# Optimization experiments

Measured on AMD Instinct MI355X. Metric: run time of the kernel, lower is better.

The kernel has to match this reference:

```python
import jax, jax.numpy as jnp
import numpy as np

B, L, H, D_IN = 64, 4096, 128, 3

def setup_inputs() -> dict:
    key = jax.random.key(0)
    ks = jax.random.split(key, 9)
    def lin_w(k, fan_in, shape):
        bound = 1.0 / np.sqrt(fan_in)
        return jax.random.uniform(k, shape, jnp.float32, -bound, bound)
    return {
        "x": jax.random.normal(ks[0], (B, L, D_IN), jnp.float32),
        "Wp": lin_w(ks[1], D_IN, (D_IN, H)), "bp": lin_w(ks[2], D_IN, (H,)),
        "Wz": lin_w(ks[3], H, (H, H)),      "bz": lin_w(ks[4], H, (H,)),
        "Wh": lin_w(ks[5], H, (H, H)),      "bh": lin_w(ks[6], H, (H,)),
        "Wg": lin_w(ks[7], H, (H, 1)),      "bg": lin_w(ks[8], H, (1,)),
    }

def reference(x, Wp, bp, Wz, bz, Wh, bh, Wg, bg):
    # Batched projections across all timesteps (B, L, H)
    inp = x @ Wp + bp                      # input_proj
    z = jax.nn.sigmoid(inp @ Wz + bz)      # update gate
    h_tilde = jnp.tanh(inp @ Wh + bh)      # candidate
    # Linear recurrence h_t = a_t * h_{t-1} + b_t, h_{-1} = 0
    a = 1.0 - z
    b = z * h_tilde
    def combine(c1, c2):
        a1, b1 = c1
        a2, b2 = c2
        return (a1 * a2, b1 * a2 + b2)
    _, h = jax.lax.associative_scan(combine, (a, b), axis=1)  # h_t (since h_{-1}=0)
    # Readout uses h BEFORE the update at each step: preds_t = gauss_head(h_{t-1})
    h_prev = jnp.concatenate([jnp.zeros_like(h[:, :1]), h[:, :-1]], axis=1)
    preds = h_prev @ Wg + bg               # (B, L, 1)
    return preds
```

## Files before the change

kernel.cpp:

```cpp
#include <hip/hip_runtime.h>
#include <hip/hip_bf16.h>
#include <stdint.h>

#define B_   64
#define L_   4096
#define H_   128
#define T_   64
#define C_   (L_/T_)
#define BH_  (B_*H_)
#define PADI 136

typedef __attribute__((ext_vector_type(8))) short short8;
typedef __attribute__((ext_vector_type(4))) short short4v;
typedef __attribute__((ext_vector_type(4))) float floatx4;
typedef __attribute__((ext_vector_type(2))) float floatx2;

#define LOG2E 1.44269504088896340736f

__device__ __forceinline__ unsigned short f2bf(float f){
    unsigned int u = __float_as_uint(f);
    u += 0x7FFFu + ((u >> 16) & 1u);
    return (unsigned short)(u >> 16);
}
__device__ __forceinline__ float bf2f(unsigned short s){
    return __uint_as_float(((unsigned int)s) << 16);
}

__global__ void prep_w(const float* __restrict__ Wz, const float* __restrict__ Wh,
                       unsigned short* __restrict__ WzT, unsigned short* __restrict__ WhT){
    int b = blockIdx.x;
    const float* W = (b < 16) ? Wz : Wh;
    unsigned short* WT = (b < 16) ? WzT : WhT;
    int b16 = b & 15, tid = threadIdx.x;
    #pragma unroll
    for (int it = 0; it < 4; ++it){
        int idx = b16*1024 + it*256 + tid;
        int n = idx >> 7, k = idx & 127;
        WT[idx] = f2bf(W[k*H_ + n]);
    }
}

__global__ __launch_bounds__(256, 4)
void carry_kogge(const floatx2* __restrict__ agg2, float* __restrict__ carry_g){
    const int row  = blockIdx.x*4 + (threadIdx.x >> 6);
    const int lane = threadIdx.x & 63;
    floatx2 v = agg2[(size_t)row*C_ + lane];
    #pragma unroll
    for (int d = 1; d < 64; d <<= 1){
        float oA = __shfl_up(v[0], d, 64);
        float oH = __shfl_up(v[1], d, 64);
        if (lane >= d){
            v[1] = fmaf(oH, v[0], v[1]);
            v[0] = oA * v[0];
        }
    }
    float eh = __shfl_up(v[1], 1, 64);
    carry_g[(size_t)row*C_ + lane] = (lane == 0) ? 0.0f : eh;
}


__global__ __launch_bounds__(256, 4)
void gates_agg(const float* __restrict__ x,
               const float* __restrict__ Wp, const float* __restrict__ bp,
               const float* __restrict__ bz, const float* __restrict__ bh,
               const float* __restrict__ Wg,
               const unsigned short* __restrict__ WzT,
               const unsigned short* __restrict__ WhT,
               floatx2* __restrict__ agg2,
               float* __restrict__ sloc, unsigned short* __restrict__ pw_g)
{
    __shared__ __align__(16) unsigned short s_ab[H_*H_];
    __shared__ float s_bz[H_], s_bh[H_], s_wg[H_];
    __shared__ float s_part[256];
    unsigned short* inp_lds = s_ab;

    const int bid = blockIdx.x;
    const int bb  = bid / C_;
    const int cc  = bid % C_;
    const int t0g = cc * T_;
    const int tid = threadIdx.x;
    const int wv = tid >> 6, lane = tid & 63, quad = lane >> 4, l15 = lane & 15;

    if (tid < H_){ s_bz[tid] = bz[tid]; s_bh[tid] = bh[tid]; s_wg[tid] = Wg[tid]; }

    {
        const int h0 = (tid & 15) * 8;
        float w0[8], w1[8], w2[8], b0[8];
        #pragma unroll
        for (int m = 0; m < 8; ++m){
            w0[m] = Wp[h0+m]; w1[m] = Wp[H_+h0+m]; w2[m] = Wp[2*H_+h0+m];
            b0[m] = bp[h0+m];
        }
        #pragma unroll
        for (int it = 0; it < 4; ++it){
            int t = (tid >> 4) + it*16;
            const float* xr = x + ((size_t)bb*L_ + t0g + t)*3;
            float x0 = xr[0], x1 = xr[1], x2 = xr[2];
            short8 pk;
            #pragma unroll
            for (int m = 0; m < 8; ++m){
                float v = b0[m];
                v = fmaf(x0, w0[m], v);
                v = fmaf(x1, w1[m], v);
                v = fmaf(x2, w2[m], v);
                pk[m] = (short)f2bf(v);
            }
            *(short8*)&inp_lds[t*PADI + h0] = pk;
        }
    }
    __syncthreads();

    const int ct0 = wv*2;

    floatx4 accz[4][2];
    #pragma unroll
    for (int r = 0; r < 4; ++r)
        #pragma unroll
        for (int c = 0; c < 2; ++c) accz[r][c] = (floatx4){0.f,0.f,0.f,0.f};
    #pragma unroll
    for (int kk = 0; kk < 4; ++kk){
        short8 af[4], bfr[2];
        #pragma unroll
        for (int r = 0; r < 4; ++r)
            af[r] = *(const short8*)&inp_lds[(r*16 + l15)*PADI + kk*32 + quad*8];
        #pragma unroll
        for (int c = 0; c < 2; ++c)
            bfr[c] = *(const short8*)&WzT[((ct0+c)*16 + l15)*H_ + kk*32 + quad*8];
        #pragma unroll
        for (int r = 0; r < 4; ++r)
            #pragma unroll
            for (int c = 0; c < 2; ++c)
                accz[r][c] = __builtin_amdgcn_mfma_f32_16x16x32_bf16(af[r], bfr[c], accz[r][c], 0, 0, 0);
    }

    floatx4 acch[4][2];
    #pragma unroll
    for (int r = 0; r < 4; ++r)
        #pragma unroll
        for (int c = 0; c < 2; ++c) acch[r][c] = (floatx4){0.f,0.f,0.f,0.f};
    #pragma unroll
    for (int kk = 0; kk < 4; ++kk){
        short8 af[4], bfr[2];
        #pragma unroll
        for (int r = 0; r < 4; ++r)
            af[r] = *(const short8*)&inp_lds[(r*16 + l15)*PADI + kk*32 + quad*8];
        #pragma unroll
        for (int c = 0; c < 2; ++c)
            bfr[c] = *(const short8*)&WhT[((ct0+c)*16 + l15)*H_ + kk*32 + quad*8];
        #pragma unroll
        for (int r = 0; r < 4; ++r)
            #pragma unroll
            for (int c = 0; c < 2; ++c)
                acch[r][c] = __builtin_amdgcn_mfma_f32_16x16x32_bf16(af[r], bfr[c], acch[r][c], 0, 0, 0);
    }
    __syncthreads();

    #pragma unroll
    for (int r = 0; r < 4; ++r){
        #pragma unroll
        for (int c = 0; c < 2; ++c){
            int col = (ct0+c)*16 + l15;
            float vbz = s_bz[col], vbh = s_bh[col];
            short8 pk;
            #pragma unroll
            for (int e = 0; e < 4; ++e){
                float szb = accz[r][c][e] + vbz;
                float a = __builtin_amdgcn_rcpf(1.0f + __builtin_amdgcn_exp2f(szb * LOG2E));
                unsigned short abf = f2bf(a);
                float af_ = bf2f(abf);
                float z = 1.0f - af_;
                float shb = acch[r][c][e] + vbh;
                float e2 = __builtin_amdgcn_exp2f(2.0f*LOG2E*fabsf(shb));
                float tt = 1.0f - 2.0f*__builtin_amdgcn_rcpf(e2 + 1.0f);
                float bt = z * copysignf(tt, shb);
                pk[2*e]   = (short)abf;
                pk[2*e+1] = (short)f2bf(bt);
            }
            int ch = (r*4 + quad) ^ l15;
            *(short8*)&s_ab[col*H_ + ch*8] = pk;
        }
    }
    __syncthreads();

    if (tid < H_){
        float A = 1.0f, h = 0.0f;
        float wgv = s_wg[tid];
        #pragma unroll
        for (int t4 = 0; t4 < 16; ++t4){
            int base = tid*H_ + ((t4 ^ (tid & 15)) << 3);
            short8 pr = *(const short8*)&s_ab[base];
            short8 wb;
            #pragma unroll
            for (int e = 0; e < 4; ++e){
                float aa = bf2f((unsigned short)pr[2*e]);
                float bv = bf2f((unsigned short)pr[2*e+1]);
                wb[2*e]   = (short)f2bf(h * wgv);
                wb[2*e+1] = (short)f2bf(A * wgv);
                A *= aa;
                h = fmaf(aa, h, bv);
            }
            *(short8*)&s_ab[base] = wb;
        }
        agg2[(size_t)(bb*H_ + tid)*C_ + cc] = (floatx2){A, h};
    }
    __syncthreads();

    {
        unsigned short* dst = pw_g + (size_t)bid*(T_*H_);
        #pragma unroll
        for (int i = 0; i < 8; ++i){
            int idx = i*256 + tid;
            int col = idx >> 4, t4 = idx & 15;
            short8 pr = *(const short8*)&s_ab[col*H_ + ((t4 ^ (col & 15)) << 3)];
            short4v pw4;
            pw4[0] = pr[1]; pw4[1] = pr[3]; pw4[2] = pr[5]; pw4[3] = pr[7];
            *(short4v*)&dst[col*T_ + t4*4] = pw4;
        }
    }

    {
        int t = tid & 63, w4 = tid >> 6;
        int t4 = t >> 2, e2 = (t & 3)*2;
        float s = 0.0f;
        #pragma unroll
        for (int j = 0; j < 32; ++j){
            int col = w4*32 + j;
            s += bf2f(s_ab[col*H_ + ((t4 ^ (col & 15)) << 3) + e2]);
        }
        s_part[w4*64 + t] = s;
    }
    __syncthreads();
    if (tid < 64)
        sloc[(size_t)bid*T_ + tid] =
            s_part[tid] + s_part[64+tid] + s_part[128+tid] + s_part[192+tid];
}

__global__ __launch_bounds__(256, 4)
void apply2(const unsigned short* __restrict__ pw_g,
            const float* __restrict__ carry_g,
            const float* __restrict__ sloc, const float* __restrict__ bg,
            float* __restrict__ preds)
{
    __shared__ float s_c[H_];
    __shared__ float s_part[256];
    const int bid = blockIdx.x;
    const int bb  = bid / C_;
    const int cc  = bid % C_;
    const int t0g = cc * T_;
    const int tid = threadIdx.x;
    const int wv = tid >> 6, lane = tid & 63;

    if (tid < H_) s_c[tid] = carry_g[(size_t)(bb*H_ + tid)*C_ + cc];
    __syncthreads();

    {
        const unsigned short* src = pw_g + (size_t)bid*(T_*H_);
        const int cl = lane >> 3, t8 = lane & 7;
        float s8[8];
        #pragma unroll
        for (int e = 0; e < 8; ++e) s8[e] = 0.0f;
        #pragma unroll
        for (int g = 0; g < 4; ++g){
            int col = wv*32 + g*8 + cl;
            short8 pw8 = *(const short8*)&src[col*T_ + t8*8];
            float cv = s_c[col];
            #pragma unroll
            for (int e = 0; e < 8; ++e)
                s8[e] = fmaf(cv, bf2f((unsigned short)pw8[e]), s8[e]);
        }
        #pragma unroll
        for (int d = 8; d < 64; d <<= 1)
            #pragma unroll
            for (int e = 0; e < 8; ++e)
                s8[e] += __shfl_xor(s8[e], d, 64);
        if (lane < 8){
            #pragma unroll
            for (int e = 0; e < 8; ++e)
                s_part[wv*64 + t8*8 + e] = s8[e];
        }
    }
    __syncthreads();
    if (tid < 64){
        float s = s_part[tid] + s_part[64+tid] + s_part[128+tid] + s_part[192+tid];
        preds[(size_t)bb*L_ + t0g + tid] = s + sloc[(size_t)bid*T_ + tid] + bg[0];
    }
}

extern "C" void kernel_launch(void* const* d_in, const int* in_sizes, int n_in,
                              void* d_out, int out_size, void* d_ws, size_t ws_size,
                              hipStream_t stream){
    const float* x  = (const float*)d_in[0];
    const float* Wp = (const float*)d_in[1];
    const float* bp = (const float*)d_in[2];
    const float* Wz = (const float*)d_in[3];
    const float* bz = (const float*)d_in[4];
    const float* Wh = (const float*)d_in[5];
    const float* bh = (const float*)d_in[6];
    const float* Wg = (const float*)d_in[7];
    const float* bg = (const float*)d_in[8];
    float* preds = (float*)d_out;

    uint8_t* w8 = (uint8_t*)d_ws;
    unsigned short* WzT = (unsigned short*)(w8);
    unsigned short* WhT = (unsigned short*)(w8 + 32768);
    floatx2* agg2 = (floatx2*)(w8 + 65536);
    float* sloc   = (float*)(w8 + 65536 + 8u*BH_*C_);
    float* carry  = (float*)(w8 + 65536 + 12u*BH_*C_);
    unsigned short* pw_g = (unsigned short*)(w8 + 65536 + 16u*BH_*C_);

    hipLaunchKernelGGL(prep_w, dim3(32), dim3(256), 0, stream, Wz, Wh, WzT, WhT);
    hipLaunchKernelGGL(gates_agg, dim3(B_*C_), dim3(256), 0, stream,
                       x, Wp, bp, bz, bh, Wg, WzT, WhT, agg2, sloc, pw_g);
    hipLaunchKernelGGL(carry_kogge, dim3(BH_/4), dim3(256), 0, stream, agg2, carry);
    hipLaunchKernelGGL(apply2, dim3(B_*C_), dim3(256), 0, stream,
                       pw_g, carry, sloc, bg, preds);
}
```

Measured before the change: 157.0 us.

## Interleave z/h MFMA loops, simplify gate math, and batch four chunks per apply block

The two separate MFMA loops for the update gate and candidate now share a single pass over the LDS A fragments, halving A-fragment loads and interleaving independent MFMA chains. The gate epilogue drops the bf16 round-trip of a before computing z and uses a direct tanh formula without fabs/copysign, which risks overflow to inf for large inputs (still yielding correct saturation via rcp). The apply2 kernel processes four chunks per block, launching a quarter as many blocks and coalescing carry loads, at the cost of less parallelism per launch.

```diff
diff --git a/kernel.cpp b/kernel.cpp
--- a/kernel.cpp
+++ b/kernel.cpp
@@ -112,46 +112,32 @@
 
     const int ct0 = wv*2;
 
-    floatx4 accz[4][2];
+    floatx4 accz[4][2], acch[4][2];
     #pragma unroll
     for (int r = 0; r < 4; ++r)
         #pragma unroll
-        for (int c = 0; c < 2; ++c) accz[r][c] = (floatx4){0.f,0.f,0.f,0.f};
+        for (int c = 0; c < 2; ++c){
+            accz[r][c] = (floatx4){0.f,0.f,0.f,0.f};
+            acch[r][c] = (floatx4){0.f,0.f,0.f,0.f};
+        }
     #pragma unroll
     for (int kk = 0; kk < 4; ++kk){
-        short8 af[4], bfr[2];
+        short8 af[4], bz_[2], bh_[2];
         #pragma unroll
         for (int r = 0; r < 4; ++r)
             af[r] = *(const short8*)&inp_lds[(r*16 + l15)*PADI + kk*32 + quad*8];
         #pragma unroll
-        for (int c = 0; c < 2; ++c)
-            bfr[c] = *(const short8*)&WzT[((ct0+c)*16 + l15)*H_ + kk*32 + quad*8];
+        for (int c = 0; c < 2; ++c){
+            bz_[c] = *(const short8*)&WzT[((ct0+c)*16 + l15)*H_ + kk*32 + quad*8];
+            bh_[c] = *(const short8*)&WhT[((ct0+c)*16 + l15)*H_ + kk*32 + quad*8];
+        }
         #pragma unroll
         for (int r = 0; r < 4; ++r)
             #pragma unroll
-            for (int c = 0; c < 2; ++c)
-                accz[r][c] = __builtin_amdgcn_mfma_f32_16x16x32_bf16(af[r], bfr[c], accz[r][c], 0, 0, 0);
-    }
-
-    floatx4 acch[4][2];
-    #pragma unroll
-    for (int r = 0; r < 4; ++r)
-        #pragma unroll
-        for (int c = 0; c < 2; ++c) acch[r][c] = (floatx4){0.f,0.f,0.f,0.f};
-    #pragma unroll
-    for (int kk = 0; kk < 4; ++kk){
-        short8 af[4], bfr[2];
-        #pragma unroll
-        for (int r = 0; r < 4; ++r)
-            af[r] = *(const short8*)&inp_lds[(r*16 + l15)*PADI + kk*32 + quad*8];
-        #pragma unroll
-        for (int c = 0; c < 2; ++c)
-            bfr[c] = *(const short8*)&WhT[((ct0+c)*16 + l15)*H_ + kk*32 + quad*8];
-        #pragma unroll
-        for (int r = 0; r < 4; ++r)
-            #pragma unroll
-            for (int c = 0; c < 2; ++c)
-                acch[r][c] = __builtin_amdgcn_mfma_f32_16x16x32_bf16(af[r], bfr[c], acch[r][c], 0, 0, 0);
+            for (int c = 0; c < 2; ++c){
+                accz[r][c] = __builtin_amdgcn_mfma_f32_16x16x32_bf16(af[r], bz_[c], accz[r][c], 0, 0, 0);
+                acch[r][c] = __builtin_amdgcn_mfma_f32_16x16x32_bf16(af[r], bh_[c], acch[r][c], 0, 0, 0);
+            }
     }
     __syncthreads();
 
@@ -166,14 +152,11 @@
             for (int e = 0; e < 4; ++e){
                 float szb = accz[r][c][e] + vbz;
                 float a = __builtin_amdgcn_rcpf(1.0f + __builtin_amdgcn_exp2f(szb * LOG2E));
-                unsigned short abf = f2bf(a);
-                float af_ = bf2f(abf);
-                float z = 1.0f - af_;
                 float shb = acch[r][c][e] + vbh;
-                float e2 = __builtin_amdgcn_exp2f(2.0f*LOG2E*fabsf(shb));
-                float tt = 1.0f - 2.0f*__builtin_amdgcn_rcpf(e2 + 1.0f);
-                float bt = z * copysignf(tt, shb);
-                pk[2*e]   = (short)abf;
+                float ex = __builtin_amdgcn_exp2f(2.0f*LOG2E*shb);
+                float th = 1.0f - 2.0f*__builtin_amdgcn_rcpf(ex + 1.0f);
+                float bt = (1.0f - a) * th;
+                pk[2*e]   = (short)f2bf(a);
                 pk[2*e+1] = (short)f2bf(bt);
             }
             int ch = (r*4 + quad) ^ l15;
@@ -241,21 +224,26 @@
             const float* __restrict__ sloc, const float* __restrict__ bg,
             float* __restrict__ preds)
 {
-    __shared__ float s_c[H_];
-    __shared__ float s_part[256];
+    __shared__ float s_c[4][H_];
+    __shared__ float s_part[4][256];
     const int bid = blockIdx.x;
-    const int bb  = bid / C_;
-    const int cc  = bid % C_;
-    const int t0g = cc * T_;
+    const int bb  = bid >> 4;
+    const int cc0 = (bid & 15) * 4;
     const int tid = threadIdx.x;
     const int wv = tid >> 6, lane = tid & 63;
-
-    if (tid < H_) s_c[tid] = carry_g[(size_t)(bb*H_ + tid)*C_ + cc];
-    __syncthreads();
-
-    {
-        const unsigned short* src = pw_g + (size_t)bid*(T_*H_);
-        const int cl = lane >> 3, t8 = lane & 7;
+    const int cl = lane >> 3, t8 = lane & 7;
+
+    #pragma unroll
+    for (int i = 0; i < 2; ++i){
+        int idx = tid + i*256;
+        int k = idx & 3, h = idx >> 2;
+        s_c[k][h] = carry_g[(size_t)(bb*H_ + h)*C_ + cc0 + k];
+    }
+    __syncthreads();
+
+    #pragma unroll
+    for (int k = 0; k < 4; ++k){
+        const unsigned short* src = pw_g + (size_t)(bb*C_ + cc0 + k)*(T_*H_);
         float s8[8];
         #pragma unroll
         for (int e = 0; e < 8; ++e) s8[e] = 0.0f;
@@ -263,7 +251,7 @@
         for (int g = 0; g < 4; ++g){
             int col = wv*32 + g*8 + cl;
             short8 pw8 = *(const short8*)&src[col*T_ + t8*8];
-            float cv = s_c[col];
+            float cv = s_c[k][col];
             #pragma unroll
             for (int e = 0; e < 8; ++e)
                 s8[e] = fmaf(cv, bf2f((unsigned short)pw8[e]), s8[e]);
@@ -276,13 +264,17 @@
         if (lane < 8){
             #pragma unroll
             for (int e = 0; e < 8; ++e)
-                s_part[wv*64 + t8*8 + e] = s8[e];
-        }
-    }
-    __syncthreads();
-    if (tid < 64){
-        float s = s_part[tid] + s_part[64+tid] + s_part[128+tid] + s_part[192+tid];
-        preds[(size_t)bb*L_ + t0g + tid] = s + sloc[(size_t)bid*T_ + tid] + bg[0];
+                s_part[k][wv*64 + t8*8 + e] = s8[e];
+        }
+    }
+    __syncthreads();
+
+    {
+        int k = tid >> 6, t = tid & 63;
+        float s = s_part[k][t] + s_part[k][64+t] + s_part[k][128+t] + s_part[k][192+t];
+        int chunk = cc0 + k;
+        preds[(size_t)bb*L_ + chunk*T_ + t] =
+            s + sloc[(size_t)(bb*C_ + chunk)*T_ + t] + bg[0];
     }
 }
 
@@ -312,6 +304,6 @@
     hipLaunchKernelGGL(gates_agg, dim3(B_*C_), dim3(256), 0, stream,
                        x, Wp, bp, bz, bh, Wg, WzT, WhT, agg2, sloc, pw_g);
     hipLaunchKernelGGL(carry_kogge, dim3(BH_/4), dim3(256), 0, stream, agg2, carry);
-    hipLaunchKernelGGL(apply2, dim3(B_*C_), dim3(256), 0, stream,
+    hipLaunchKernelGGL(apply2, dim3(B_*C_/4), dim3(256), 0, stream,
                        pw_g, carry, sloc, bg, preds);
 }
```

Measured after the change: 154.8 us. Within noise of the previous version (-1.4%).
